# Performance work log

Hardware: AMD Instinct MI355X
Metric: run time of the kernel (lower is better)

## Reference

```python
import jax, jax.numpy as jnp
import numpy as np

B, T, E, H = 2, 2048, 1024, 16
D = E // H  # head_dim = 64


def setup_inputs() -> dict:
    key = jax.random.key(0)
    ks = jax.random.split(key, 9)
    s = 0.02
    x = jax.random.normal(ks[0], (B, T, E), dtype=jnp.float32)
    # additive causal mask, broadcastable to (B, H, T, T)
    causal = jnp.tril(jnp.ones((T, T), dtype=bool))
    uni_causal_mask = jnp.where(causal, 0.0, -1e9).astype(jnp.float32)[None, None]
    # torch Linear weights are (out_features, in_features); out = H*D, in = D
    Wq = jax.random.normal(ks[1], (H * D, D), dtype=jnp.float32) * s
    bq = jax.random.normal(ks[2], (H * D,), dtype=jnp.float32) * s
    Wk = jax.random.normal(ks[3], (H * D, D), dtype=jnp.float32) * s
    bk = jax.random.normal(ks[4], (H * D,), dtype=jnp.float32) * s
    Wv = jax.random.normal(ks[5], (H * D, D), dtype=jnp.float32) * s
    bv = jax.random.normal(ks[6], (H * D,), dtype=jnp.float32) * s
    Wp = jax.random.normal(ks[7], (E, E), dtype=jnp.float32) * s
    bp = jax.random.normal(ks[8], (E,), dtype=jnp.float32) * s
    return {"x": x, "uni_causal_mask": uni_causal_mask,
            "Wq": Wq, "bq": bq, "Wk": Wk, "bk": bk,
            "Wv": Wv, "bv": bv, "Wp": Wp, "bp": bp}


def _per_head_proj(xh, W, b):
    # xh: (B, T, H, D). Original code projects each head's D-dim slice with
    # Linear(D, H*D) and get_head_dim keeps only the diagonal block i for
    # head i, i.e. each head uses W[i*D:(i+1)*D, :] and b[i*D:(i+1)*D].
    W3 = W.reshape(H, D, D)  # (H, out D, in D)
    b2 = b.reshape(H, D)
    y = jnp.einsum('bthi,hoi->bhto', xh, W3) + b2[None, :, None, :]
    return y  # (B, H, T, D)


def reference(x, uni_causal_mask, Wq, bq, Wk, bk, Wv, bv, Wp, bp):
    b, t, e = x.shape
    xh = x.reshape(b, t, H, D)
    q = _per_head_proj(xh, Wq, bq)  # (B,H,T,D)
    k = _per_head_proj(xh, Wk, bk)
    v = _per_head_proj(xh, Wv, bv)
    scale = D ** (-0.5)
    attn = jnp.einsum('bhtd,bhsd->bhts', (q * scale).astype(jnp.float32),
                      k.astype(jnp.float32))
    attn = attn + uni_causal_mask
    attn = jax.nn.softmax(attn, axis=-1).astype(x.dtype)
    out = jnp.einsum('bhts,bhsd->bhtd', attn, v)
    out = out.transpose(0, 2, 1, 3).reshape(b, t, e)
    return out @ Wp.T + bp
```

## Files before the change

kernel.cpp:

```cpp
#include <hip/hip_runtime.h>

typedef __attribute__((ext_vector_type(4))) float f32x4;
typedef __attribute__((ext_vector_type(8))) __bf16 bf16x8;
typedef __attribute__((ext_vector_type(4))) unsigned short us4;
typedef __attribute__((ext_vector_type(8))) unsigned short us8;

#define DEVI static __device__ __forceinline__

constexpr int T_ = 2048, E_ = 1024, H_ = 16, D_ = 64;
#define QSCALE (0.125f * 1.44269504088896f)

DEVI unsigned short f2b(float f) {
  union { float fv; unsigned u; } c; c.fv = f;
  unsigned r = c.u + 0x7fffu + ((c.u >> 16) & 1u);
  return (unsigned short)(r >> 16);
}

#if __has_builtin(__builtin_amdgcn_exp2f)
DEVI float fexp2(float x) { return __builtin_amdgcn_exp2f(x); }
#else
DEVI float fexp2(float x) { return __expf(x * 0.69314718056f); }
#endif

DEVI f32x4 mfma16(bf16x8 a, bf16x8 b, f32x4 c) {
  return __builtin_amdgcn_mfma_f32_16x16x32_bf16(a, b, c, 0, 0, 0);
}

__launch_bounds__(256)
__global__ void wcvt_kernel(const float* __restrict__ Wq,
                            const float* __restrict__ Wk,
                            const float* __restrict__ Wv,
                            unsigned short* __restrict__ wqb,
                            unsigned short* __restrict__ wkb,
                            unsigned short* __restrict__ wvb)
{
  int blk = blockIdx.x;
  const float* src; unsigned short* dst; float s = 1.0f;
  if (blk < 64)       { src = Wq; dst = wqb; s = QSCALE; }
  else if (blk < 128) { src = Wk; dst = wkb; blk -= 64; }
  else                { src = Wv; dst = wvb; blk -= 128; }
  int i = blk * 256 + threadIdx.x;
  float4 v = *(const float4*)(src + (size_t)i * 4);
  us4 o; o[0] = f2b(v.x * s); o[1] = f2b(v.y * s); o[2] = f2b(v.z * s); o[3] = f2b(v.w * s);
  *(us4*)(dst + (size_t)i * 4) = o;
}

__launch_bounds__(256)
__global__ void wpcvt_kernel(const float* __restrict__ Wp,
                             unsigned short* __restrict__ wpb)
{
  int i = blockIdx.x * 256 + threadIdx.x;
  float4 v = *(const float4*)(Wp + (size_t)i * 4);
  us4 o; o[0] = f2b(v.x); o[1] = f2b(v.y); o[2] = f2b(v.z); o[3] = f2b(v.w);
  *(us4*)(wpb + (size_t)i * 4) = o;
}

__launch_bounds__(256)
__global__ void qkv_kernel(const float* __restrict__ x,
                           const unsigned short* __restrict__ wqb,
                           const float* __restrict__ bq,
                           const unsigned short* __restrict__ wkb,
                           const float* __restrict__ bk,
                           const unsigned short* __restrict__ wvb,
                           const float* __restrict__ bv,
                           unsigned short* __restrict__ qo,
                           unsigned short* __restrict__ ko,
                           unsigned short* __restrict__ vto)
{
  const int bh = blockIdx.x;
  const int b  = bh >> 4;
  const int h  = bh & (H_ - 1);
  const int t0 = blockIdx.y * 128;
  __shared__ unsigned short Xl[128][72];
  __shared__ unsigned short Wl[3][64][72];
  const int tid = threadIdx.x;

  #pragma unroll
  for (int p = 0; p < 8; ++p) {
    int idx = p * 256 + tid;
    int row = idx >> 4, c4 = idx & 15;
    const float* gp = x + ((size_t)(b * T_ + t0 + row)) * E_ + h * 64 + c4 * 4;
    float4 v = *(const float4*)gp;
    us4 o; o[0] = f2b(v.x); o[1] = f2b(v.y); o[2] = f2b(v.z); o[3] = f2b(v.w);
    *(us4*)&Xl[row][c4 * 4] = o;
  }
  {
    const unsigned short* wsrc0 = wqb + (size_t)h * 4096;
    const unsigned short* wsrc1 = wkb + (size_t)h * 4096;
    const unsigned short* wsrc2 = wvb + (size_t)h * 4096;
    #pragma unroll
    for (int p = 0; p < 2; ++p) {
      int idx = p * 256 + tid;
      int row = idx >> 3, c8 = (idx & 7) * 8;
      *(us8*)&Wl[0][row][c8] = *(const us8*)(wsrc0 + row * 64 + c8);
      *(us8*)&Wl[1][row][c8] = *(const us8*)(wsrc1 + row * 64 + c8);
      *(us8*)&Wl[2][row][c8] = *(const us8*)(wsrc2 + row * 64 + c8);
    }
  }
  __syncthreads();

  const int w = tid >> 6, lane = tid & 63, lo = lane & 15, g = lane >> 4;
  const int tl0 = w * 32;

  bf16x8 xb[2][2];
  #pragma unroll
  for (int tt = 0; tt < 2; ++tt)
    #pragma unroll
    for (int kd = 0; kd < 2; ++kd)
      xb[tt][kd] = *(const bf16x8*)&Xl[tl0 + tt * 16 + lo][kd * 32 + g * 8];

  #pragma unroll
  for (int tsel = 0; tsel < 2; ++tsel) {
    const float* bias = tsel ? bk : bq;
    unsigned short* outp = tsel ? ko : qo;
    const float bs = tsel ? 1.0f : QSCALE;
    #pragma unroll
    for (int ot = 0; ot < 4; ++ot) {
      bf16x8 a0 = *(const bf16x8*)&Wl[tsel][ot * 16 + lo][g * 8];
      bf16x8 a1 = *(const bf16x8*)&Wl[tsel][ot * 16 + lo][32 + g * 8];
      float4 bv4 = *(const float4*)(bias + h * 64 + ot * 16 + g * 4);
      float bb[4] = {bv4.x * bs, bv4.y * bs, bv4.z * bs, bv4.w * bs};
      #pragma unroll
      for (int tt = 0; tt < 2; ++tt) {
        f32x4 acc = {0.f, 0.f, 0.f, 0.f};
        acc = mfma16(a0, xb[tt][0], acc);
        acc = mfma16(a1, xb[tt][1], acc);
        int tg = t0 + tl0 + tt * 16 + lo;
        us4 pk;
        #pragma unroll
        for (int r = 0; r < 4; ++r) pk[r] = f2b(acc[r] + bb[r]);
        *(us4*)(outp + ((size_t)(bh * T_ + tg)) * 64 + ot * 16 + g * 4) = pk;
      }
    }
  }

  #pragma unroll
  for (int rt = 0; rt < 2; ++rt) {
    bf16x8 a0 = *(const bf16x8*)&Xl[tl0 + rt * 16 + lo][g * 8];
    bf16x8 a1 = *(const bf16x8*)&Xl[tl0 + rt * 16 + lo][32 + g * 8];
    #pragma unroll
    for (int ct = 0; ct < 4; ++ct) {
      bf16x8 b0 = *(const bf16x8*)&Wl[2][ct * 16 + lo][g * 8];
      bf16x8 b1 = *(const bf16x8*)&Wl[2][ct * 16 + lo][32 + g * 8];
      f32x4 acc = {0.f, 0.f, 0.f, 0.f};
      acc = mfma16(a0, b0, acc);
      acc = mfma16(a1, b1, acc);
      int d = ct * 16 + lo;
      float bvs = bv[h * 64 + d];
      int tg = t0 + tl0 + rt * 16 + g * 4;
      us4 pk;
      #pragma unroll
      for (int r = 0; r < 4; ++r) pk[r] = f2b(acc[r] + bvs);
      *(us4*)(vto + ((size_t)(bh * 64 + d)) * T_ + tg) = pk;
    }
  }
}

__launch_bounds__(256)
__global__ void flash_kernel(const unsigned short* __restrict__ q,
                             const unsigned short* __restrict__ kk_,
                             const unsigned short* __restrict__ vt,
                             unsigned short* __restrict__ ao)
{
  const int bh = blockIdx.x;
  const int b = bh >> 4, h = bh & 15;
  __shared__ unsigned short Kl[2][64][64];
  __shared__ unsigned short Vl[2][64][64];
  __shared__ unsigned short Pl[4][16][64];
  const int tid = threadIdx.x, w = tid >> 6, lane = tid & 63, lo = lane & 15, g = lane >> 4;
  const int rs = lo & 7;

  const int srow = tid >> 3, sgi = tid & 7;
  const int sgis = (sgi ^ (srow & 7)) * 8;
  const unsigned short* kbase = kk_ + ((size_t)bh * T_ + srow) * 64 + sgi * 8;
  const unsigned short* vbase = vt + ((size_t)(bh * 64 + srow)) * T_ + sgi * 8;

  #pragma unroll 1
  for (int half = 0; half < 2; ++half) {
    const int qt = half ? (31 - blockIdx.y) : blockIdx.y;
    const int t0 = qt * 64;
    const int tw = t0 + w * 16;

    bf16x8 qf[2];
    const unsigned short* qb = q + ((size_t)(bh * T_ + tw + lo)) * 64;
    #pragma unroll
    for (int kd = 0; kd < 2; ++kd)
      qf[kd] = *(const bf16x8*)(qb + kd * 32 + g * 8);

    float m_ = -1e30f, l_ = 0.f;
    f32x4 zero4 = {0.f, 0.f, 0.f, 0.f};
    f32x4 oacc[4];
    #pragma unroll
    for (int dt = 0; dt < 4; ++dt) oacc[dt] = zero4;

    const int nsteps = qt + 1;
    us8 kr0 = *(const us8*)(kbase);
    us8 kr1 = *(const us8*)(kbase + 2048);
    us8 vr0 = *(const us8*)(vbase);
    us8 vr1 = *(const us8*)(vbase + (size_t)32 * T_);
    *(us8*)&Kl[0][srow][sgis] = kr0;
    *(us8*)&Kl[0][srow + 32][sgis] = kr1;
    *(us8*)&Vl[0][srow][sgis] = vr0;
    *(us8*)&Vl[0][srow + 32][sgis] = vr1;
    if (nsteps > 1) {
      kr0 = *(const us8*)(kbase + 4096);
      kr1 = *(const us8*)(kbase + 4096 + 2048);
      vr0 = *(const us8*)(vbase + 64);
      vr1 = *(const us8*)(vbase + 64 + (size_t)32 * T_);
    }
    __syncthreads();

    for (int stp = 0; stp < nsteps; ++stp) {
      const int s0 = stp * 64;
      const int cur = stp & 1;
      us8 nk0, nk1, nv0, nv1;
      const bool pf = (stp + 2 < nsteps);
      if (pf) {
        const size_t ko_ = (size_t)(stp + 2) * 4096;
        nk0 = *(const us8*)(kbase + ko_);
        nk1 = *(const us8*)(kbase + ko_ + 2048);
        nv0 = *(const us8*)(vbase + (stp + 2) * 64);
        nv1 = *(const us8*)(vbase + (stp + 2) * 64 + (size_t)32 * T_);
      }
      {
        f32x4 sacc[4];
        #pragma unroll
        for (int ss = 0; ss < 4; ++ss) sacc[ss] = zero4;
        __builtin_amdgcn_s_setprio(1);
        #pragma unroll
        for (int ss = 0; ss < 4; ++ss) {
          bf16x8 ka0 = *(const bf16x8*)&Kl[cur][ss * 16 + lo][(g ^ rs) * 8];
          bf16x8 ka1 = *(const bf16x8*)&Kl[cur][ss * 16 + lo][((g | 4) ^ rs) * 8];
          sacc[ss] = mfma16(ka0, qf[0], sacc[ss]);
          sacc[ss] = mfma16(ka1, qf[1], sacc[ss]);
        }
        __builtin_amdgcn_s_setprio(0);
        if (s0 + 63 > tw) {
          #pragma unroll
          for (int ss = 0; ss < 4; ++ss)
            #pragma unroll
            for (int r = 0; r < 4; ++r) {
              int sg = s0 + ss * 16 + g * 4 + r;
              if (sg > tw + lo) sacc[ss][r] = -1e30f;
            }
        }
        float mx = -1e30f;
        #pragma unroll
        for (int ss = 0; ss < 4; ++ss)
          #pragma unroll
          for (int r = 0; r < 4; ++r) mx = fmaxf(mx, sacc[ss][r]);
        mx = fmaxf(mx, __shfl_xor(mx, 16));
        mx = fmaxf(mx, __shfl_xor(mx, 32));
        float mn = fmaxf(m_, mx);
        float corr = fexp2(m_ - mn);
        m_ = mn;
        float sum = 0.f;
        #pragma unroll
        for (int ss = 0; ss < 4; ++ss) {
          us4 pk;
          #pragma unroll
          for (int r = 0; r < 4; ++r) {
            float pv = fexp2(sacc[ss][r] - mn);
            sum += pv;
            pk[r] = f2b(pv);
          }
          *(us4*)&Pl[w][lo][(((ss * 2 + (g >> 1)) ^ rs) << 3) + (g & 1) * 4] = pk;
        }
        sum += __shfl_xor(sum, 16);
        sum += __shfl_xor(sum, 32);
        l_ = l_ * corr + sum;
        #pragma unroll
        for (int dt = 0; dt < 4; ++dt) oacc[dt] *= corr;
        __builtin_amdgcn_s_setprio(1);
        #pragma unroll
        for (int kh = 0; kh < 2; ++kh) {
          bf16x8 pb = *(const bf16x8*)&Pl[w][lo][((kh * 4 + g) ^ rs) * 8];
          #pragma unroll
          for (int dt = 0; dt < 4; ++dt) {
            bf16x8 va = *(const bf16x8*)&Vl[cur][dt * 16 + lo][((kh * 4 + g) ^ rs) * 8];
            oacc[dt] = mfma16(va, pb, oacc[dt]);
          }
        }
        __builtin_amdgcn_s_setprio(0);
      }
      if (stp + 1 < nsteps) {
        *(us8*)&Kl[cur ^ 1][srow][sgis] = kr0;
        *(us8*)&Kl[cur ^ 1][srow + 32][sgis] = kr1;
        *(us8*)&Vl[cur ^ 1][srow][sgis] = vr0;
        *(us8*)&Vl[cur ^ 1][srow + 32][sgis] = vr1;
      }
      __syncthreads();
      if (pf) { kr0 = nk0; kr1 = nk1; vr0 = nv0; vr1 = nv1; }
    }
    float inv = 1.0f / l_;
    unsigned short* op = ao + ((size_t)(b * T_ + tw + lo)) * E_ + h * 64;
    #pragma unroll
    for (int dt = 0; dt < 4; ++dt) {
      us4 pk;
      #pragma unroll
      for (int r = 0; r < 4; ++r) pk[r] = f2b(oacc[dt][r] * inv);
      *(us4*)(op + dt * 16 + g * 4) = pk;
    }
  }
}

__launch_bounds__(256)
__global__ void proj_kernel(const unsigned short* __restrict__ ao,
                            const unsigned short* __restrict__ wpb,
                            const float* __restrict__ bp,
                            float* __restrict__ out)
{
  const int m0 = blockIdx.x * 128;
  const int n0 = blockIdx.y * 64;
  __shared__ unsigned short Al[2][128][40];
  __shared__ unsigned short Bl[2][64][40];
  const int tid = threadIdx.x, w = tid >> 6, lane = tid & 63, lo = lane & 15, g = lane >> 4;
  const int wr = (w >> 1) * 64, wc = (w & 1) * 32;
  f32x4 zero4 = {0.f, 0.f, 0.f, 0.f};
  f32x4 acc[4][2];
  #pragma unroll
  for (int i = 0; i < 4; ++i)
    #pragma unroll
    for (int j = 0; j < 2; ++j) acc[i][j] = zero4;

  const int arow = tid >> 1, acol = (tid & 1) * 16;
  const int brow = tid >> 2, bcol = (tid & 3) * 8;
  const unsigned short* abase = ao + (size_t)(m0 + arow) * 1024 + acol;
  const unsigned short* bbase = wpb + (size_t)(n0 + brow) * 1024 + bcol;

  us8 a0 = *(const us8*)(abase);
  us8 a1 = *(const us8*)(abase + 8);
  us8 b0 = *(const us8*)(bbase);
  *(us8*)&Al[0][arow][acol] = a0;
  *(us8*)&Al[0][arow][acol + 8] = a1;
  *(us8*)&Bl[0][brow][bcol] = b0;
  a0 = *(const us8*)(abase + 32);
  a1 = *(const us8*)(abase + 40);
  b0 = *(const us8*)(bbase + 32);
  __syncthreads();

  for (int it = 0; it < 32; ++it) {
    const int cur = it & 1;
    us8 na0, na1, nb0;
    const bool pf = (it + 2 < 32);
    if (pf) {
      const int kn = (it + 2) * 32;
      na0 = *(const us8*)(abase + kn);
      na1 = *(const us8*)(abase + kn + 8);
      nb0 = *(const us8*)(bbase + kn);
    }
    bf16x8 af[4], bfr[2];
    #pragma unroll
    for (int i = 0; i < 4; ++i) af[i] = *(const bf16x8*)&Al[cur][wr + i * 16 + lo][g * 8];
    #pragma unroll
    for (int j = 0; j < 2; ++j) bfr[j] = *(const bf16x8*)&Bl[cur][wc + j * 16 + lo][g * 8];
    __builtin_amdgcn_s_setprio(1);
    #pragma unroll
    for (int i = 0; i < 4; ++i)
      #pragma unroll
      for (int j = 0; j < 2; ++j)
        acc[i][j] = mfma16(af[i], bfr[j], acc[i][j]);
    __builtin_amdgcn_s_setprio(0);
    if (it + 1 < 32) {
      *(us8*)&Al[cur ^ 1][arow][acol] = a0;
      *(us8*)&Al[cur ^ 1][arow][acol + 8] = a1;
      *(us8*)&Bl[cur ^ 1][brow][bcol] = b0;
    }
    __syncthreads();
    if (pf) { a0 = na0; a1 = na1; b0 = nb0; }
  }
  #pragma unroll
  for (int j = 0; j < 2; ++j) {
    int n = n0 + wc + j * 16 + lo;
    float bias = bp[n];
    #pragma unroll
    for (int i = 0; i < 4; ++i) {
      #pragma unroll
      for (int r = 0; r < 4; ++r)
        out[(size_t)(m0 + wr + i * 16 + g * 4 + r) * 1024 + n] = acc[i][j][r] + bias;
    }
  }
}

extern "C" void kernel_launch(void* const* d_in, const int* in_sizes, int n_in,
                              void* d_out, int out_size, void* d_ws, size_t ws_size,
                              hipStream_t stream)
{
  const float* x  = (const float*)d_in[0];
  const float* Wq = (const float*)d_in[2];
  const float* bq = (const float*)d_in[3];
  const float* Wk = (const float*)d_in[4];
  const float* bk = (const float*)d_in[5];
  const float* Wv = (const float*)d_in[6];
  const float* bv = (const float*)d_in[7];
  const float* Wp = (const float*)d_in[8];
  const float* bp = (const float*)d_in[9];
  float* out = (float*)d_out;

  char* ws = (char*)d_ws;
  const size_t SZ = (size_t)2 * 16 * 2048 * 64 * 2;
  unsigned short* q  = (unsigned short*)(ws);
  unsigned short* kb = (unsigned short*)(ws + SZ);
  unsigned short* vt = (unsigned short*)(ws + 2 * SZ);
  unsigned short* ao = (unsigned short*)(ws + 3 * SZ);
  unsigned short* wqb = ao;
  unsigned short* wkb = ao + 65536;
  unsigned short* wvb = ao + 131072;
  unsigned short* wpb = q;

  wcvt_kernel<<<dim3(192), 256, 0, stream>>>(Wq, Wk, Wv, wqb, wkb, wvb);
  qkv_kernel<<<dim3(32, 16), 256, 0, stream>>>(x, wqb, bq, wkb, bk, wvb, bv, q, kb, vt);
  flash_kernel<<<dim3(32, 16), 256, 0, stream>>>(q, kb, vt, ao);
  wpcvt_kernel<<<dim3(1024), 256, 0, stream>>>(Wp, wpb);
  proj_kernel<<<dim3(32, 16), 256, 0, stream>>>(ao, wpb, bp, out);
}
```

Before: 89.05 us.

## Software-pipeline PV MMA one step behind QK and add lazy softmax rescale

Restructures the flash attention loop so the P·V MFMAs for the previous key block are issued right after the current block's Q·K MFMAs. V moves to a triple-buffered LDS ring so the older V tile stays readable while the next one is written. Adds a conditional online-softmax rescale that only runs when the running max grows by more than 8 (log2 units), plus a diagonal-only causal mask check and a hardware bf16 conversion. These aim to overlap matrix work with the softmax math and cut the per-step rescale cost, at the price of more LDS, more registers and an extra barrier.

```diff
diff --git a/kernel.cpp b/kernel.cpp
--- a/kernel.cpp
+++ b/kernel.cpp
@@ -11,9 +11,7 @@
 #define QSCALE (0.125f * 1.44269504088896f)
 
 DEVI unsigned short f2b(float f) {
-  union { float fv; unsigned u; } c; c.fv = f;
-  unsigned r = c.u + 0x7fffu + ((c.u >> 16) & 1u);
-  return (unsigned short)(r >> 16);
+  union { __bf16 b; unsigned short u; } c; c.b = (__bf16)f; return c.u;
 }
 
 #if __has_builtin(__builtin_amdgcn_exp2f)
@@ -79,8 +77,7 @@
   for (int p = 0; p < 8; ++p) {
     int idx = p * 256 + tid;
     int row = idx >> 4, c4 = idx & 15;
-    const float* gp = x + ((size_t)(b * T_ + t0 + row)) * E_ + h * 64 + c4 * 4;
-    float4 v = *(const float4*)gp;
+    float4 v = *(const float4*)(x + ((size_t)(b * T_ + t0 + row)) * E_ + h * 64 + c4 * 4);
     us4 o; o[0] = f2b(v.x); o[1] = f2b(v.y); o[2] = f2b(v.z); o[3] = f2b(v.w);
     *(us4*)&Xl[row][c4 * 4] = o;
   }
@@ -165,7 +162,7 @@
   const int bh = blockIdx.x;
   const int b = bh >> 4, h = bh & 15;
   __shared__ unsigned short Kl[2][64][64];
-  __shared__ unsigned short Vl[2][64][64];
+  __shared__ unsigned short Vl[3][64][64];
   __shared__ unsigned short Pl[4][16][64];
   const int tid = threadIdx.x, w = tid >> 6, lane = tid & 63, lo = lane & 15, g = lane >> 4;
   const int rs = lo & 7;
@@ -198,6 +195,7 @@
     us8 kr1 = *(const us8*)(kbase + 2048);
     us8 vr0 = *(const us8*)(vbase);
     us8 vr1 = *(const us8*)(vbase + (size_t)32 * T_);
+    __syncthreads();
     *(us8*)&Kl[0][srow][sgis] = kr0;
     *(us8*)&Kl[0][srow + 32][sgis] = kr1;
     *(us8*)&Vl[0][srow][sgis] = vr0;
@@ -210,8 +208,10 @@
     }
     __syncthreads();
 
+    bf16x8 pb[2];
+    int vprev = 0;
+
     for (int stp = 0; stp < nsteps; ++stp) {
-      const int s0 = stp * 64;
       const int cur = stp & 1;
       us8 nk0, nk1, nv0, nv1;
       const bool pf = (stp + 2 < nsteps);
@@ -222,76 +222,90 @@
         nv0 = *(const us8*)(vbase + (stp + 2) * 64);
         nv1 = *(const us8*)(vbase + (stp + 2) * 64 + (size_t)32 * T_);
       }
-      {
-        f32x4 sacc[4];
-        #pragma unroll
-        for (int ss = 0; ss < 4; ++ss) sacc[ss] = zero4;
-        __builtin_amdgcn_s_setprio(1);
-        #pragma unroll
-        for (int ss = 0; ss < 4; ++ss) {
-          bf16x8 ka0 = *(const bf16x8*)&Kl[cur][ss * 16 + lo][(g ^ rs) * 8];
-          bf16x8 ka1 = *(const bf16x8*)&Kl[cur][ss * 16 + lo][((g | 4) ^ rs) * 8];
-          sacc[ss] = mfma16(ka0, qf[0], sacc[ss]);
-          sacc[ss] = mfma16(ka1, qf[1], sacc[ss]);
+      f32x4 sacc[4];
+      #pragma unroll
+      for (int ss = 0; ss < 4; ++ss) sacc[ss] = zero4;
+      __builtin_amdgcn_s_setprio(1);
+      #pragma unroll
+      for (int ss = 0; ss < 4; ++ss) {
+        bf16x8 ka0 = *(const bf16x8*)&Kl[cur][ss * 16 + lo][(g ^ rs) * 8];
+        bf16x8 ka1 = *(const bf16x8*)&Kl[cur][ss * 16 + lo][((g | 4) ^ rs) * 8];
+        sacc[ss] = mfma16(ka0, qf[0], sacc[ss]);
+        sacc[ss] = mfma16(ka1, qf[1], sacc[ss]);
+      }
+      if (stp > 0) {
+        #pragma unroll
+        for (int kh = 0; kh < 2; ++kh) {
+          #pragma unroll
+          for (int dt = 0; dt < 4; ++dt) {
+            bf16x8 va = *(const bf16x8*)&Vl[vprev][dt * 16 + lo][((kh * 4 + g) ^ rs) * 8];
+            oacc[dt] = mfma16(va, pb[kh], oacc[dt]);
+          }
         }
-        __builtin_amdgcn_s_setprio(0);
-        if (s0 + 63 > tw) {
-          #pragma unroll
-          for (int ss = 0; ss < 4; ++ss)
-            #pragma unroll
-            for (int r = 0; r < 4; ++r) {
-              int sg = s0 + ss * 16 + g * 4 + r;
-              if (sg > tw + lo) sacc[ss][r] = -1e30f;
-            }
-        }
-        float mx = -1e30f;
+      }
+      __builtin_amdgcn_s_setprio(0);
+      if (stp == nsteps - 1) {
         #pragma unroll
         for (int ss = 0; ss < 4; ++ss)
           #pragma unroll
-          for (int r = 0; r < 4; ++r) mx = fmaxf(mx, sacc[ss][r]);
-        mx = fmaxf(mx, __shfl_xor(mx, 16));
-        mx = fmaxf(mx, __shfl_xor(mx, 32));
+          for (int r = 0; r < 4; ++r) {
+            int sg = t0 + ss * 16 + g * 4 + r;
+            if (sg > tw + lo) sacc[ss][r] = -1e30f;
+          }
+      }
+      float mx = -1e30f;
+      #pragma unroll
+      for (int ss = 0; ss < 4; ++ss)
+        #pragma unroll
+        for (int r = 0; r < 4; ++r) mx = fmaxf(mx, sacc[ss][r]);
+      mx = fmaxf(mx, __shfl_xor(mx, 16));
+      mx = fmaxf(mx, __shfl_xor(mx, 32));
+      if (!__all(mx <= m_ + 8.0f)) {
         float mn = fmaxf(m_, mx);
         float corr = fexp2(m_ - mn);
         m_ = mn;
-        float sum = 0.f;
-        #pragma unroll
-        for (int ss = 0; ss < 4; ++ss) {
-          us4 pk;
-          #pragma unroll
-          for (int r = 0; r < 4; ++r) {
-            float pv = fexp2(sacc[ss][r] - mn);
-            sum += pv;
-            pk[r] = f2b(pv);
-          }
-          *(us4*)&Pl[w][lo][(((ss * 2 + (g >> 1)) ^ rs) << 3) + (g & 1) * 4] = pk;
+        l_ *= corr;
+        #pragma unroll
+        for (int dt = 0; dt < 4; ++dt) oacc[dt] *= corr;
+      }
+      float sum = 0.f;
+      #pragma unroll
+      for (int ss = 0; ss < 4; ++ss) {
+        us4 pk;
+        #pragma unroll
+        for (int r = 0; r < 4; ++r) {
+          float pv = fexp2(sacc[ss][r] - m_);
+          sum += pv;
+          pk[r] = f2b(pv);
         }
-        sum += __shfl_xor(sum, 16);
-        sum += __shfl_xor(sum, 32);
-        l_ = l_ * corr + sum;
-        #pragma unroll
-        for (int dt = 0; dt < 4; ++dt) oacc[dt] *= corr;
-        __builtin_amdgcn_s_setprio(1);
-        #pragma unroll
-        for (int kh = 0; kh < 2; ++kh) {
-          bf16x8 pb = *(const bf16x8*)&Pl[w][lo][((kh * 4 + g) ^ rs) * 8];
-          #pragma unroll
-          for (int dt = 0; dt < 4; ++dt) {
-            bf16x8 va = *(const bf16x8*)&Vl[cur][dt * 16 + lo][((kh * 4 + g) ^ rs) * 8];
-            oacc[dt] = mfma16(va, pb, oacc[dt]);
-          }
-        }
-        __builtin_amdgcn_s_setprio(0);
-      }
+        *(us4*)&Pl[w][lo][(((ss * 2 + (g >> 1)) ^ rs) << 3) + (g & 1) * 4] = pk;
+      }
+      sum += __shfl_xor(sum, 16);
+      sum += __shfl_xor(sum, 32);
+      l_ += sum;
+      pb[0] = *(const bf16x8*)&Pl[w][lo][(g ^ rs) * 8];
+      pb[1] = *(const bf16x8*)&Pl[w][lo][((4 + g) ^ rs) * 8];
+      vprev = stp % 3;
       if (stp + 1 < nsteps) {
         *(us8*)&Kl[cur ^ 1][srow][sgis] = kr0;
         *(us8*)&Kl[cur ^ 1][srow + 32][sgis] = kr1;
-        *(us8*)&Vl[cur ^ 1][srow][sgis] = vr0;
-        *(us8*)&Vl[cur ^ 1][srow + 32][sgis] = vr1;
+        const int vn = (stp + 1) % 3;
+        *(us8*)&Vl[vn][srow][sgis] = vr0;
+        *(us8*)&Vl[vn][srow + 32][sgis] = vr1;
       }
       __syncthreads();
       if (pf) { kr0 = nk0; kr1 = nk1; vr0 = nv0; vr1 = nv1; }
     }
+    __builtin_amdgcn_s_setprio(1);
+    #pragma unroll
+    for (int kh = 0; kh < 2; ++kh) {
+      #pragma unroll
+      for (int dt = 0; dt < 4; ++dt) {
+        bf16x8 va = *(const bf16x8*)&Vl[vprev][dt * 16 + lo][((kh * 4 + g) ^ rs) * 8];
+        oacc[dt] = mfma16(va, pb[kh], oacc[dt]);
+      }
+    }
+    __builtin_amdgcn_s_setprio(0);
     float inv = 1.0f / l_;
     unsigned short* op = ao + ((size_t)(b * T_ + tw + lo)) * E_ + h * 64;
     #pragma unroll
```

New measurement: 84.03 us. -5.6%, faster.
